# Optimization experiments

Hardware: AMD Instinct MI355X
Metric: run time of the kernel (lower is better)

Reference implementation:

```python
import jax, jax.numpy as jnp
import numpy as np

NUM_GATES = 8192
INPUT_SIZE = 8192
BATCH = 2048
TEMPERATURE = 1.0


def setup_inputs() -> dict:
    key = jax.random.key(0)
    k1, k2 = jax.random.split(key)
    x = jax.random.uniform(k1, (BATCH, INPUT_SIZE), dtype=jnp.float32)
    # Per-gate logits; torch init is zeros with logits[3]=logits[5]=2.0, but any
    # values exercise the same math — use small random logits for a nontrivial softmax.
    gate_logits = jax.random.normal(k2, (NUM_GATES, 16), dtype=jnp.float32)
    return {"x": x, "gate_logits": gate_logits}


def _soft_ops(a, b):
    # a, b: [B, G] clamped to [0,1]. Returns [B, G, 16] continuous logic ops.
    a = jnp.clip(a, 0.0, 1.0)
    b = jnp.clip(b, 0.0, 1.0)
    ab = a * b
    one = jnp.ones_like(a)
    zero = jnp.zeros_like(a)
    return jnp.stack([
        zero,                 # 0: FALSE
        ab,                   # 1: a AND b
        a - ab,               # 2: a AND NOT b
        a,                    # 3: a
        b - ab,               # 4: NOT a AND b
        b,                    # 5: b
        a + b - 2 * ab,       # 6: XOR
        a + b - ab,           # 7: OR
        1 - (a + b - ab),     # 8: NOR
        1 - (a + b - 2 * ab), # 9: XNOR
        1 - b,                # 10: NOT b
        1 - b + ab,           # 11: a OR NOT b
        1 - a,                # 12: NOT a
        1 - a + ab,           # 13: NOT a OR b
        1 - ab,               # 14: NAND
        one,                  # 15: TRUE
    ], axis=-1)


def reference(x, gate_logits):
    G = gate_logits.shape[0]
    gi = jnp.arange(G)
    idx1 = gi % INPUT_SIZE              # input1 for gate i
    idx2 = (gi + 1) % INPUT_SIZE        # input2 for gate i (input_size > 1)
    a = x[:, idx1]                      # [B, G]
    b = x[:, idx2]                      # [B, G]
    ops = _soft_ops(a, b)               # [B, G, 16]
    probs = jax.nn.softmax(gate_logits / TEMPERATURE, axis=-1)  # [G, 16]
    return jnp.einsum("bgo,go->bg", ops, probs)  # [B, G]
```

## Files before the change

### kernel.cpp

```cpp
#include <hip/hip_runtime.h>
#include <math.h>


constexpr int INPUT_SIZE = 8192;
constexpr int NUM_GATES  = 8192;
constexpr int BATCH      = 2048;
constexpr int V4_PER_ROW = INPUT_SIZE / 4;

__global__ __launch_bounds__(256) void gate_weights_kernel(
    const float* __restrict__ logits, float4* __restrict__ w) {
    int g = blockIdx.x * blockDim.x + threadIdx.x;
    if (g >= NUM_GATES) return;

    const float4* lp = reinterpret_cast<const float4*>(logits + (size_t)g * 16);
    float4 l0 = lp[0], l1 = lp[1], l2 = lp[2], l3 = lp[3];
    float p[16];
    p[0]=l0.x;  p[1]=l0.y;  p[2]=l0.z;  p[3]=l0.w;
    p[4]=l1.x;  p[5]=l1.y;  p[6]=l1.z;  p[7]=l1.w;
    p[8]=l2.x;  p[9]=l2.y;  p[10]=l2.z; p[11]=l2.w;
    p[12]=l3.x; p[13]=l3.y; p[14]=l3.z; p[15]=l3.w;

    float m = p[0];
    #pragma unroll
    for (int i = 1; i < 16; ++i) m = fmaxf(m, p[i]);
    float s = 0.f;
    #pragma unroll
    for (int i = 0; i < 16; ++i) { p[i] = __expf(p[i] - m); s += p[i]; }
    float inv = 1.f / s;
    #pragma unroll
    for (int i = 0; i < 16; ++i) p[i] *= inv;

    float c0  = p[8]+p[9]+p[10]+p[11]+p[12]+p[13]+p[14]+p[15];
    float ca  = p[2]+p[3]+p[6]+p[7] - p[8]-p[9]-p[12]-p[13];
    float cb  = p[4]+p[5]+p[6]+p[7] - p[8]-p[9]-p[10]-p[11];
    float cab = p[1]-p[2]-p[4]-2.f*p[6]-p[7]+p[8]+2.f*p[9]+p[11]+p[13]-p[14];

    w[g] = make_float4(c0, ca, cb, cab);
}

__global__ __launch_bounds__(256) void dll_main_kernel(
    const float* __restrict__ x,
    const float4* __restrict__ w,
    float* __restrict__ out) {

    int tid  = blockIdx.x * blockDim.x + threadIdx.x;
    int col4 = tid & (V4_PER_ROW - 1);
    int row0 = tid >> 11;

    int g = col4 * 4;
    float4 w0 = w[g + 0];
    float4 w1 = w[g + 1];
    float4 w2 = w[g + 2];
    float4 w3 = w[g + 3];

    const float4* x4  = reinterpret_cast<const float4*>(x);
    float4*      out4 = reinterpret_cast<float4*>(out);
    int col4n = (col4 + 1) & (V4_PER_ROW - 1);

    for (int row = row0; row < BATCH; row += 256) {
        size_t base = (size_t)row * V4_PER_ROW;
        float4 xv = x4[base + col4];
        float4 xn = x4[base + col4n];

        float a0 = fminf(fmaxf(xv.x, 0.f), 1.f);
        float a1 = fminf(fmaxf(xv.y, 0.f), 1.f);
        float a2 = fminf(fmaxf(xv.z, 0.f), 1.f);
        float a3 = fminf(fmaxf(xv.w, 0.f), 1.f);
        float a4 = fminf(fmaxf(xn.x, 0.f), 1.f);

        float4 o;
        o.x = fmaf(w0.w, a0 * a1, fmaf(w0.z, a1, fmaf(w0.y, a0, w0.x)));
        o.y = fmaf(w1.w, a1 * a2, fmaf(w1.z, a2, fmaf(w1.y, a1, w1.x)));
        o.z = fmaf(w2.w, a2 * a3, fmaf(w2.z, a3, fmaf(w2.y, a2, w2.x)));
        o.w = fmaf(w3.w, a3 * a4, fmaf(w3.z, a4, fmaf(w3.y, a3, w3.x)));

        out4[base + col4] = o;
    }
}

extern "C" void kernel_launch(void* const* d_in, const int* in_sizes, int n_in,
                              void* d_out, int out_size, void* d_ws, size_t ws_size,
                              hipStream_t stream) {
    const float* x      = reinterpret_cast<const float*>(d_in[0]);
    const float* logits = reinterpret_cast<const float*>(d_in[1]);
    float*       out    = reinterpret_cast<float*>(d_out);
    float4*      w      = reinterpret_cast<float4*>(d_ws);

    gate_weights_kernel<<<NUM_GATES / 256, 256, 0, stream>>>(logits, w);

    int total_threads = BATCH / 8 * V4_PER_ROW;
    dll_main_kernel<<<total_threads / 256, 256, 0, stream>>>(x, w, out);
}
```

Before: 31.46 us.

## Fuse gate softmax into main kernel and use nontemporal output stores

Removes the separate gate-weight kernel and computes each thread's four softmax-derived affine coefficients directly from the logits inside the main kernel. This eliminates one launch and the workspace write/read. The grid is halved so each thread processes more rows with an unrolled loop, and output stores become nontemporal. The trade-off is redundant softmax computation across the threads sharing a column.

```diff
diff --git a/kernel.cpp b/kernel.cpp
--- a/kernel.cpp
+++ b/kernel.cpp
@@ -3,17 +3,16 @@
 
 
 constexpr int INPUT_SIZE = 8192;
-constexpr int NUM_GATES  = 8192;
 constexpr int BATCH      = 2048;
 constexpr int V4_PER_ROW = INPUT_SIZE / 4;
+constexpr int NBLOCKS    = 1024;
+constexpr int ROW_STRIDE = 128;
 
-__global__ __launch_bounds__(256) void gate_weights_kernel(
-    const float* __restrict__ logits, float4* __restrict__ w) {
-    int g = blockIdx.x * blockDim.x + threadIdx.x;
-    if (g >= NUM_GATES) return;
+typedef float floatx4 __attribute__((ext_vector_type(4)));
 
-    const float4* lp = reinterpret_cast<const float4*>(logits + (size_t)g * 16);
-    float4 l0 = lp[0], l1 = lp[1], l2 = lp[2], l3 = lp[3];
+__device__ __forceinline__ floatx4 softmax_affine(const float* __restrict__ logits, int g) {
+    const floatx4* lp = reinterpret_cast<const floatx4*>(logits + (size_t)g * 16);
+    floatx4 l0 = lp[0], l1 = lp[1], l2 = lp[2], l3 = lp[3];
     float p[16];
     p[0]=l0.x;  p[1]=l0.y;  p[2]=l0.z;  p[3]=l0.w;
     p[4]=l1.x;  p[5]=l1.y;  p[6]=l1.z;  p[7]=l1.w;
@@ -27,20 +26,18 @@
     #pragma unroll
     for (int i = 0; i < 16; ++i) { p[i] = __expf(p[i] - m); s += p[i]; }
     float inv = 1.f / s;
-    #pragma unroll
-    for (int i = 0; i < 16; ++i) p[i] *= inv;
 
     float c0  = p[8]+p[9]+p[10]+p[11]+p[12]+p[13]+p[14]+p[15];
     float ca  = p[2]+p[3]+p[6]+p[7] - p[8]-p[9]-p[12]-p[13];
     float cb  = p[4]+p[5]+p[6]+p[7] - p[8]-p[9]-p[10]-p[11];
     float cab = p[1]-p[2]-p[4]-2.f*p[6]-p[7]+p[8]+2.f*p[9]+p[11]+p[13]-p[14];
-
-    w[g] = make_float4(c0, ca, cb, cab);
+    floatx4 w = { c0*inv, ca*inv, cb*inv, cab*inv };
+    return w;
 }
 
-__global__ __launch_bounds__(256) void dll_main_kernel(
+__global__ __launch_bounds__(256) void dll_fused_kernel(
     const float* __restrict__ x,
-    const float4* __restrict__ w,
+    const float* __restrict__ logits,
     float* __restrict__ out) {
 
     int tid  = blockIdx.x * blockDim.x + threadIdx.x;
@@ -48,19 +45,20 @@
     int row0 = tid >> 11;
 
     int g = col4 * 4;
-    float4 w0 = w[g + 0];
-    float4 w1 = w[g + 1];
-    float4 w2 = w[g + 2];
-    float4 w3 = w[g + 3];
+    floatx4 w0 = softmax_affine(logits, g + 0);
+    floatx4 w1 = softmax_affine(logits, g + 1);
+    floatx4 w2 = softmax_affine(logits, g + 2);
+    floatx4 w3 = softmax_affine(logits, g + 3);
 
-    const float4* x4  = reinterpret_cast<const float4*>(x);
-    float4*      out4 = reinterpret_cast<float4*>(out);
+    const floatx4* x4  = reinterpret_cast<const floatx4*>(x);
+    floatx4*      out4 = reinterpret_cast<floatx4*>(out);
     int col4n = (col4 + 1) & (V4_PER_ROW - 1);
 
-    for (int row = row0; row < BATCH; row += 256) {
+    #pragma unroll 4
+    for (int row = row0; row < BATCH; row += ROW_STRIDE) {
         size_t base = (size_t)row * V4_PER_ROW;
-        float4 xv = x4[base + col4];
-        float4 xn = x4[base + col4n];
+        floatx4 xv = x4[base + col4];
+        floatx4 xn = x4[base + col4n];
 
         float a0 = fminf(fmaxf(xv.x, 0.f), 1.f);
         float a1 = fminf(fmaxf(xv.y, 0.f), 1.f);
@@ -68,13 +66,13 @@
         float a3 = fminf(fmaxf(xv.w, 0.f), 1.f);
         float a4 = fminf(fmaxf(xn.x, 0.f), 1.f);
 
-        float4 o;
+        floatx4 o;
         o.x = fmaf(w0.w, a0 * a1, fmaf(w0.z, a1, fmaf(w0.y, a0, w0.x)));
         o.y = fmaf(w1.w, a1 * a2, fmaf(w1.z, a2, fmaf(w1.y, a1, w1.x)));
         o.z = fmaf(w2.w, a2 * a3, fmaf(w2.z, a3, fmaf(w2.y, a2, w2.x)));
         o.w = fmaf(w3.w, a3 * a4, fmaf(w3.z, a4, fmaf(w3.y, a3, w3.x)));
 
-        out4[base + col4] = o;
+        __builtin_nontemporal_store(o, &out4[base + col4]);
     }
 }
 
@@ -84,10 +82,6 @@
     const float* x      = reinterpret_cast<const float*>(d_in[0]);
     const float* logits = reinterpret_cast<const float*>(d_in[1]);
     float*       out    = reinterpret_cast<float*>(d_out);
-    float4*      w      = reinterpret_cast<float4*>(d_ws);
 
-    gate_weights_kernel<<<NUM_GATES / 256, 256, 0, stream>>>(logits, w);
-
-    int total_threads = BATCH / 8 * V4_PER_ROW;
-    dll_main_kernel<<<total_threads / 256, 256, 0, stream>>>(x, w, out);
+    dll_fused_kernel<<<NBLOCKS, 256, 0, stream>>>(x, logits, out);
 }
```

Result: slower. 34.07 us (+8.3%).
